# Performance work log

Measured on AMD Instinct MI355X. Metric: run time of the kernel, lower is better.

The kernel has to match this reference:

```python
import jax, jax.numpy as jnp
import numpy as np

N = 100000   # nodes per ntype
E = 1600000  # edges per etype (avg degree 16)
D = 128      # in_channels == hid_channels
LN_EPS = 1e-5


def setup_inputs() -> dict:
    key = jax.random.key(0)
    k = jax.random.split(key, 16)
    scale = 1.0 / np.sqrt(D)
    inp = {
        "x_A": jax.random.normal(k[0], (N, D), jnp.float32),
        "x_B": jax.random.normal(k[1], (N, D), jnp.float32),
        # per-etype GraphConv weights, etype order: [aa, ab, ba, bb]
        "W0": jax.random.normal(k[2], (4, D, D), jnp.float32) * scale,
        "b0": jnp.zeros((4, D), jnp.float32),
        "W1": jax.random.normal(k[3], (4, D, D), jnp.float32) * scale,
        "b1": jnp.zeros((4, D), jnp.float32),
        # LayerNorm params: [layer, ntype(A=0,B=1), D]
        "ln_gamma": jnp.ones((2, 2, D), jnp.float32),
        "ln_beta": jnp.zeros((2, 2, D), jnp.float32),
        "src_aa": jax.random.randint(k[4], (E,), 0, N, jnp.int32),
        "dst_aa": jax.random.randint(k[5], (E,), 0, N, jnp.int32),
        "src_ab": jax.random.randint(k[6], (E,), 0, N, jnp.int32),
        "dst_ab": jax.random.randint(k[7], (E,), 0, N, jnp.int32),
        "src_ba": jax.random.randint(k[8], (E,), 0, N, jnp.int32),
        "dst_ba": jax.random.randint(k[9], (E,), 0, N, jnp.int32),
        "src_bb": jax.random.randint(k[10], (E,), 0, N, jnp.int32),
        "dst_bb": jax.random.randint(k[11], (E,), 0, N, jnp.int32),
    }
    return inp


def _layer_norm(x, g, b):
    m = jnp.mean(x, axis=-1, keepdims=True)
    v = jnp.var(x, axis=-1, keepdims=True)
    return (x - m) * jax.lax.rsqrt(v + LN_EPS) * g + b


def _graph_conv(x, W, b, src, dst, n_dst, act):
    # dgl GraphConv norm='both': D_dst^{-1/2} A D_src^{-1/2} X W + b
    deg_out = jnp.clip(jax.ops.segment_sum(jnp.ones_like(src, x.dtype), src, num_segments=x.shape[0]), 1.0)
    deg_in = jnp.clip(jax.ops.segment_sum(jnp.ones_like(dst, x.dtype), dst, num_segments=n_dst), 1.0)
    h = (x * jax.lax.rsqrt(deg_out)[:, None]) @ W            # transform first (in==out)
    agg = jax.ops.segment_sum(h[src], dst, num_segments=n_dst)
    out = agg * jax.lax.rsqrt(deg_in)[:, None] + b
    return jax.nn.relu(out) if act else out


def reference(x_A, x_B, W0, b0, W1, b1, ln_gamma, ln_beta,
              src_aa, dst_aa, src_ab, dst_ab, src_ba, dst_ba, src_bb, dst_bb):
    hA, hB = x_A, x_B
    for l, (W, bias) in enumerate([(W0, b0), (W1, b1)]):
        act = (l == 0)  # relu inside each GraphConv for all but the last layer
        # HeteroGraphConv aggregate='sum': sum per-relation (activated) outputs per dst ntype
        nA = _graph_conv(hA, W[0], bias[0], src_aa, dst_aa, N, act) + \
             _graph_conv(hB, W[2], bias[2], src_ba, dst_ba, N, act)
        nB = _graph_conv(hA, W[1], bias[1], src_ab, dst_ab, N, act) + \
             _graph_conv(hB, W[3], bias[3], src_bb, dst_bb, N, act)
        hA = _layer_norm(nA, ln_gamma[l, 0], ln_beta[l, 0])
        hB = _layer_norm(nB, ln_gamma[l, 1], ln_beta[l, 1])
        # dropout p=0.0 (eval) -> identity
    return jnp.stack([hA, hB])  # [ntype, N, D]
```

## Files before the change

kernel.cpp:

```cpp
#include <hip/hip_runtime.h>
#include <hip/hip_bf16.h>

#define D 128
typedef unsigned int uint;
typedef unsigned short ushort;
typedef unsigned char uchar;
typedef short short8 __attribute__((ext_vector_type(8)));
typedef float f32x4 __attribute__((ext_vector_type(4)));

#define BKT_SHIFT 8
#define NBMAX 512
#define PART_EPT 16
#define EPB 4096
#define SCAT_CAP 8192

__device__ __forceinline__ ushort f2bf(float f) {
    uint u = __float_as_uint(f);
    return (ushort)((u + 0x7fffu + ((u >> 16) & 1u)) >> 16);
}
__device__ __forceinline__ float bf2f(uint s) { return __uint_as_float(s << 16); }

__global__ __launch_bounds__(256) void bhist4_k(
    const int* __restrict__ s0, const int* __restrict__ d0,
    const int* __restrict__ s1, const int* __restrict__ d1,
    const int* __restrict__ s2, const int* __restrict__ d2,
    const int* __restrict__ s3, const int* __restrict__ d3,
    int* __restrict__ bcs, int* __restrict__ bcd, int N, int E) {
    const int e = blockIdx.y;
    const int* sp = e == 0 ? s0 : e == 1 ? s1 : e == 2 ? s2 : s3;
    const int* dp = e == 0 ? d0 : e == 1 ? d1 : e == 2 ? d2 : d3;
    const int NB = (N + 255) >> BKT_SHIFT;
    __shared__ int hs[NBMAX], hd[NBMAX];
    for (int j = threadIdx.x; j < NBMAX; j += 256) { hs[j] = 0; hd[j] = 0; }
    __syncthreads();
    const int base = blockIdx.x * 8192;
#pragma unroll
    for (int k = 0; k < 8; ++k) {
        int idx = base + (k * 256 + threadIdx.x) * 4;
        if (idx + 4 <= E) {
            int4 s = *(const int4*)(sp + idx);
            int4 d = *(const int4*)(dp + idx);
            atomicAdd(&hs[s.x >> BKT_SHIFT], 1); atomicAdd(&hs[s.y >> BKT_SHIFT], 1);
            atomicAdd(&hs[s.z >> BKT_SHIFT], 1); atomicAdd(&hs[s.w >> BKT_SHIFT], 1);
            atomicAdd(&hd[d.x >> BKT_SHIFT], 1); atomicAdd(&hd[d.y >> BKT_SHIFT], 1);
            atomicAdd(&hd[d.z >> BKT_SHIFT], 1); atomicAdd(&hd[d.w >> BKT_SHIFT], 1);
        } else {
            for (int i = idx; i < E && i < idx + 4; ++i) {
                atomicAdd(&hs[sp[i] >> BKT_SHIFT], 1);
                atomicAdd(&hd[dp[i] >> BKT_SHIFT], 1);
            }
        }
    }
    __syncthreads();
    for (int j = threadIdx.x; j < NB; j += 256) {
        if (hs[j]) atomicAdd(&bcs[e * NBMAX + j], hs[j]);
        if (hd[j]) atomicAdd(&bcd[e * NBMAX + j], hd[j]);
    }
}

__global__ __launch_bounds__(512) void bscan_k(
    const int* __restrict__ bcs, const int* __restrict__ bcd,
    int* __restrict__ sbase, int* __restrict__ scur,
    int* __restrict__ dbase, int* __restrict__ dcur, int N) {
    const int e = blockIdx.y;
    const int side = blockIdx.x;
    const int NB = (N + 255) >> BKT_SHIFT;
    const int* in = (side ? bcd : bcs) + e * NBMAX;
    int* b0 = (side ? dbase : sbase) + e * NBMAX;
    int* c0 = (side ? dcur : scur) + e * NBMAX;
    const int tid = threadIdx.x, lane = tid & 63, wid = tid >> 6;
    int v = (tid < NB) ? in[tid] : 0;
    int x = v;
#pragma unroll
    for (int off = 1; off < 64; off <<= 1) {
        int t = __shfl_up(x, off);
        if (lane >= off) x += t;
    }
    __shared__ int ws[8];
    if (lane == 63) ws[wid] = x;
    __syncthreads();
    if (tid == 0) {
        int run = 0;
#pragma unroll
        for (int w = 0; w < 8; ++w) { int t = ws[w]; ws[w] = run; run += t; }
    }
    __syncthreads();
    int excl = ws[wid] + x - v;
    if (tid < NB) { b0[tid] = excl; c0[tid] = excl; }
}

__device__ __forceinline__ void scan_reserve(int* h, int* gcur, int* Lb, int* Gb,
                                             int* ws) {
    const int t = threadIdx.x, lane = t & 63, wid = t >> 6;
    int c0 = h[2 * t], c1 = h[2 * t + 1];
    int tsum = c0 + c1;
    int x = tsum;
#pragma unroll
    for (int off = 1; off < 64; off <<= 1) {
        int u = __shfl_up(x, off);
        if (lane >= off) x += u;
    }
    if (lane == 63) ws[wid] = x;
    __syncthreads();
    if (t == 0) {
        int run = 0;
#pragma unroll
        for (int w = 0; w < 4; ++w) { int u = ws[w]; ws[w] = run; run += u; }
    }
    __syncthreads();
    int excl = ws[wid] + x - tsum;
    Lb[2 * t] = excl;
    Lb[2 * t + 1] = excl + c0;
    Gb[2 * t] = c0 ? atomicAdd(&gcur[2 * t], c0) : 0;
    Gb[2 * t + 1] = c1 ? atomicAdd(&gcur[2 * t + 1], c1) : 0;
}

__global__ __launch_bounds__(256) void part4_k(
    const int* __restrict__ s0, const int* __restrict__ d0,
    const int* __restrict__ s1, const int* __restrict__ d1,
    const int* __restrict__ s2, const int* __restrict__ d2,
    const int* __restrict__ s3, const int* __restrict__ d3,
    int* __restrict__ scur, int* __restrict__ dcur,
    uint* __restrict__ pd, uchar* __restrict__ ps, int N, int E) {
    const int e = blockIdx.y;
    const int* sp = e == 0 ? s0 : e == 1 ? s1 : e == 2 ? s2 : s3;
    const int* dp = e == 0 ? d0 : e == 1 ? d1 : e == 2 ? d2 : d3;
    uint* ptd = pd + (size_t)e * E;
    uchar* pts = ps + (size_t)e * E;
    __shared__ int hd[NBMAX], hs[NBMAX];
    __shared__ int Lb[NBMAX], Gb[NBMAX];
    __shared__ uint rec[EPB];
    __shared__ int dst[EPB];
    __shared__ int ws[4];
    for (int j = threadIdx.x; j < NBMAX; j += 256) { hd[j] = 0; hs[j] = 0; }
    __syncthreads();
    int myd[PART_EPT], mys[PART_EPT], rkd[PART_EPT], rks[PART_EPT];
    const int base = blockIdx.x * EPB;
    const int nE = min(EPB, E - base);
#pragma unroll
    for (int k = 0; k < PART_EPT; ++k) {
        int idx = base + k * 256 + threadIdx.x;
        if (idx < E) {
            int d = dp[idx], s = sp[idx];
            myd[k] = d; mys[k] = s;
            rkd[k] = atomicAdd(&hd[d >> BKT_SHIFT], 1);
            rks[k] = atomicAdd(&hs[s >> BKT_SHIFT], 1);
        } else {
            myd[k] = -1;
        }
    }
    __syncthreads();
    scan_reserve(hd, dcur + e * NBMAX, Lb, Gb, ws);
    __syncthreads();
#pragma unroll
    for (int k = 0; k < PART_EPT; ++k) {
        if (myd[k] >= 0) {
            int b = myd[k] >> BKT_SHIFT;
            int q = Lb[b] + rkd[k];
            rec[q] = ((uint)(myd[k] & 255) << 24) | (uint)mys[k];
            dst[q] = Gb[b] + rkd[k];
        }
    }
    __syncthreads();
    for (int i = threadIdx.x; i < nE; i += 256) ptd[dst[i]] = rec[i];
    __syncthreads();
    scan_reserve(hs, scur + e * NBMAX, Lb, Gb, ws);
    __syncthreads();
#pragma unroll
    for (int k = 0; k < PART_EPT; ++k) {
        if (myd[k] >= 0) {
            int b = mys[k] >> BKT_SHIFT;
            int q = Lb[b] + rks[k];
            rec[q] = (uint)(mys[k] & 255);
            dst[q] = Gb[b] + rks[k];
        }
    }
    __syncthreads();
    for (int i = threadIdx.x; i < nE; i += 256) pts[dst[i]] = (uchar)rec[i];
}

__global__ __launch_bounds__(256) void scat4_k(
    const uint* __restrict__ pd, const int* __restrict__ dbase,
    const int* __restrict__ bcd, int* __restrict__ start_g,
    int* __restrict__ cnt_g, float* __restrict__ rs_in,
    int* __restrict__ csr, int N, int E) {
    const int e = blockIdx.y;
    const int b = blockIdx.x;
    const int node0 = b << BKT_SHIFT;
    const int nodes = min(256, N - node0);
    const uint* pt = pd + (size_t)e * E;
    int* out = csr + (size_t)e * E;
    const int csr_base = dbase[e * NBMAX + b];
    const int span = bcd[e * NBMAX + b];
    __shared__ int cnt[256];
    __shared__ int cur[256];
    __shared__ int woff[4];
    __shared__ int lcsr[SCAT_CAP];
    const int tid = threadIdx.x, lane = tid & 63, wid = tid >> 6;
    cnt[tid] = 0;
    __syncthreads();
    for (int i = tid; i < span; i += 256) atomicAdd(&cnt[pt[csr_base + i] >> 24], 1);
    __syncthreads();
    int c = cnt[tid];
    int x = c;
#pragma unroll
    for (int off = 1; off < 64; off <<= 1) {
        int t = __shfl_up(x, off);
        if (lane >= off) x += t;
    }
    if (lane == 63) woff[wid] = x;
    __syncthreads();
    if (tid == 0) {
        int run = 0;
#pragma unroll
        for (int w = 0; w < 4; ++w) { int t = woff[w]; woff[w] = run; run += t; }
    }
    __syncthreads();
    int loc = woff[wid] + x - c;
    cur[tid] = loc;
    if (tid < nodes) {
        int n = node0 + tid;
        start_g[(size_t)e * N + n] = csr_base + loc;
        cnt_g[(size_t)e * N + n] = c;
        rs_in[(size_t)e * N + n] = rsqrtf((float)max(c, 1));
    }
    __syncthreads();
    for (int i = tid; i < span; i += 256) {
        uint pk = pt[csr_base + i];
        int pos = atomicAdd(&cur[pk >> 24], 1);
        int s = (int)(pk & 0xFFFFFFu);
        if (pos < SCAT_CAP) lcsr[pos] = s;
        else out[csr_base + pos] = s;
    }
    __syncthreads();
    const int lim = span < SCAT_CAP ? span : SCAT_CAP;
    for (int i = tid; i < lim; i += 256) out[csr_base + i] = lcsr[i];
}

__global__ __launch_bounds__(256) void shist_k(
    const uchar* __restrict__ ps, const int* __restrict__ sbase,
    const int* __restrict__ bcs, float* __restrict__ rs_out, int N, int E) {
    const int e = blockIdx.y;
    const int b = blockIdx.x;
    const int node0 = b << BKT_SHIFT;
    const int nodes = min(256, N - node0);
    const uchar* pt = ps + (size_t)e * E;
    const int base = sbase[e * NBMAX + b];
    const int span = bcs[e * NBMAX + b];
    __shared__ int c[256];
    c[threadIdx.x] = 0;
    __syncthreads();
    for (int i = threadIdx.x; i < span; i += 256) atomicAdd(&c[pt[base + i]], 1);
    __syncthreads();
    if (threadIdx.x < nodes)
        rs_out[(size_t)e * N + node0 + threadIdx.x] = rsqrtf((float)max(c[threadIdx.x], 1));
}

__global__ __launch_bounds__(256) void wswz_k(const float* __restrict__ W0,
                                              const float* __restrict__ W1,
                                              ushort* __restrict__ WF) {
    int t = blockIdx.x * 256 + threadIdx.x;
    int lane = t & 63, kf = (t >> 6) & 3, ct = (t >> 8) & 7, e = (t >> 11) & 3, l = (t >> 13) & 1;
    const float* Ws = (l ? W1 : W0) + (size_t)e * D * D;
    int m = lane & 15, q = lane >> 4;
    const float* src = Ws + (size_t)(kf * 32 + q * 8) * D + ct * 16 + m;
    ushort v[8];
#pragma unroll
    for (int j = 0; j < 8; ++j) v[j] = f2bf(src[(size_t)j * D]);
    uint4 pk;
    pk.x = (uint)v[0] | ((uint)v[1] << 16);
    pk.y = (uint)v[2] | ((uint)v[3] << 16);
    pk.z = (uint)v[4] | ((uint)v[5] << 16);
    pk.w = (uint)v[6] | ((uint)v[7] << 16);
    *(uint4*)(WF + ((size_t)(l * 4 + e) * 2048 + (ct * 4 + kf) * 64 + lane) * 8) = pk;
}

__global__ __launch_bounds__(256) void gemm_pair_k(
    const float* __restrict__ XA, const float* __restrict__ XB,
    const ushort* __restrict__ WF,
    const float* __restrict__ rs,
    ushort* __restrict__ yb,
    int n) {
    const int p = blockIdx.y;
    const float* X = p ? XB : XA;
    const int e0 = 2 * p, e1 = 2 * p + 1;
    const short8* F0 = (const short8*)(WF + (size_t)e0 * 16384);
    const short8* F1 = (const short8*)(WF + (size_t)e1 * 16384);
    const float* rs0 = rs + (size_t)e0 * n;
    const float* rs1 = rs + (size_t)e1 * n;
    ushort* Y0 = yb + (size_t)e0 * n * D;
    ushort* Y1 = yb + (size_t)e1 * n * D;
    const int lane = threadIdx.x & 63;
    const int m = lane & 15, q = lane >> 4;
    const int wave = blockIdx.x * 4 + (threadIdx.x >> 6);
    const int nw = gridDim.x * 4;
    const int nstrips = (n + 15) >> 4;
    for (int sidx = wave; sidx < nstrips; sidx += nw) {
        const int r = sidx * 16 + m;
        const int rc = r < n ? r : n - 1;
        const float* xp = X + (size_t)rc * D + q * 8;
        short8 xf[4];
#pragma unroll
        for (int kf = 0; kf < 4; ++kf) {
            float4 u0 = *(const float4*)(xp + kf * 32);
            float4 u1 = *(const float4*)(xp + kf * 32 + 4);
            short8 v;
            v[0] = (short)f2bf(u0.x); v[1] = (short)f2bf(u0.y);
            v[2] = (short)f2bf(u0.z); v[3] = (short)f2bf(u0.w);
            v[4] = (short)f2bf(u1.x); v[5] = (short)f2bf(u1.y);
            v[6] = (short)f2bf(u1.z); v[7] = (short)f2bf(u1.w);
            xf[kf] = v;
        }
        f32x4 a0[8], a1[8];
#pragma unroll
        for (int ct = 0; ct < 8; ++ct) {
            a0[ct] = (f32x4){0.f, 0.f, 0.f, 0.f};
            a1[ct] = (f32x4){0.f, 0.f, 0.f, 0.f};
        }
#pragma unroll
        for (int ct = 0; ct < 8; ++ct)
#pragma unroll
            for (int kf = 0; kf < 4; ++kf) {
                a0[ct] = __builtin_amdgcn_mfma_f32_16x16x32_bf16(
                    F0[(ct * 4 + kf) * 64 + lane], xf[kf], a0[ct], 0, 0, 0);
                a1[ct] = __builtin_amdgcn_mfma_f32_16x16x32_bf16(
                    F1[(ct * 4 + kf) * 64 + lane], xf[kf], a1[ct], 0, 0, 0);
            }
        if (r < n) {
            float s0v = rs0[r], s1v = rs1[r];
            ushort* y0r = Y0 + (size_t)r * D + q * 4;
            ushort* y1r = Y1 + (size_t)r * D + q * 4;
#pragma unroll
            for (int ct = 0; ct < 8; ++ct) {
                uint2 w;
                w.x = (uint)f2bf(a0[ct][0] * s0v) | ((uint)f2bf(a0[ct][1] * s0v) << 16);
                w.y = (uint)f2bf(a0[ct][2] * s0v) | ((uint)f2bf(a0[ct][3] * s0v) << 16);
                *(uint2*)(y0r + ct * 16) = w;
                uint2 z;
                z.x = (uint)f2bf(a1[ct][0] * s1v) | ((uint)f2bf(a1[ct][1] * s1v) << 16);
                z.y = (uint)f2bf(a1[ct][2] * s1v) | ((uint)f2bf(a1[ct][3] * s1v) << 16);
                *(uint2*)(y1r + ct * 16) = z;
            }
        }
    }
}

#define ACC8(acc, u)                                                     \
    acc[0] += bf2f(u.x & 0xffffu); acc[1] += bf2f(u.x >> 16);            \
    acc[2] += bf2f(u.y & 0xffffu); acc[3] += bf2f(u.y >> 16);            \
    acc[4] += bf2f(u.z & 0xffffu); acc[5] += bf2f(u.z >> 16);            \
    acc[6] += bf2f(u.w & 0xffffu); acc[7] += bf2f(u.w >> 16);

__global__ __launch_bounds__(256) void agg_ln4_k(
    const ushort* __restrict__ yb, const int* __restrict__ csr,
    const int* __restrict__ start, const int* __restrict__ cnt,
    const float* __restrict__ rs_in, const float* __restrict__ bias,
    const float* __restrict__ lng, const float* __restrict__ lnb,
    float* __restrict__ outA, float* __restrict__ outB,
    int N, int E, int act, int layer) {
    const int dt = blockIdx.y;
    const int eA = dt, eB = dt + 2;
    const int lane = threadIdx.x & 63;
    const int grp = lane >> 4, m = lane & 15;
    const int row = blockIdx.x * 4 + (threadIdx.x >> 6);
    if (row >= N) return;
    const uint4* YA = (const uint4*)(yb + (size_t)eA * N * D);
    const uint4* YB = (const uint4*)(yb + (size_t)eB * N * D);
    const int* cAp = csr + (size_t)eA * E;
    const int* cBp = csr + (size_t)eB * E;
    int iA = start[(size_t)eA * N + row], enA = iA + cnt[(size_t)eA * N + row];
    int iB = start[(size_t)eB * N + row], enB = iB + cnt[(size_t)eB * N + row];
    float aA[8] = {0.f, 0.f, 0.f, 0.f, 0.f, 0.f, 0.f, 0.f};
    float aB[8] = {0.f, 0.f, 0.f, 0.f, 0.f, 0.f, 0.f, 0.f};
    for (; iA + 4 <= enA; iA += 4) {
        int s = cAp[iA + grp];
        uint4 u = YA[(size_t)s * 16 + m];
        ACC8(aA, u)
    }
    {
        int remA = enA - iA;
        if (grp < remA) {
            int s = cAp[iA + grp];
            uint4 u = YA[(size_t)s * 16 + m];
            ACC8(aA, u)
        }
    }
    for (; iB + 4 <= enB; iB += 4) {
        int s = cBp[iB + grp];
        uint4 u = YB[(size_t)s * 16 + m];
        ACC8(aB, u)
    }
    {
        int remB = enB - iB;
        if (grp < remB) {
            int s = cBp[iB + grp];
            uint4 u = YB[(size_t)s * 16 + m];
            ACC8(aB, u)
        }
    }
#pragma unroll
    for (int j = 0; j < 8; ++j) {
        aA[j] += __shfl_xor(aA[j], 16); aA[j] += __shfl_xor(aA[j], 32);
        aB[j] += __shfl_xor(aB[j], 16); aB[j] += __shfl_xor(aB[j], 32);
    }
    float riA = rs_in[(size_t)eA * N + row], riB = rs_in[(size_t)eB * N + row];
    float4 bA0 = *(const float4*)(bias + eA * D + m * 8);
    float4 bA1 = *(const float4*)(bias + eA * D + m * 8 + 4);
    float4 bB0 = *(const float4*)(bias + eB * D + m * 8);
    float4 bB1 = *(const float4*)(bias + eB * D + m * 8 + 4);
    float bAv[8] = {bA0.x, bA0.y, bA0.z, bA0.w, bA1.x, bA1.y, bA1.z, bA1.w};
    float bBv[8] = {bB0.x, bB0.y, bB0.z, bB0.w, bB1.x, bB1.y, bB1.z, bB1.w};
    float v[8];
#pragma unroll
    for (int j = 0; j < 8; ++j) {
        float x = fmaf(aA[j], riA, bAv[j]);
        float w = fmaf(aB[j], riB, bBv[j]);
        if (act) { x = fmaxf(x, 0.f); w = fmaxf(w, 0.f); }
        v[j] = x + w;
    }
    float s = 0.f, qq = 0.f;
#pragma unroll
    for (int j = 0; j < 8; ++j) { s += v[j]; qq += v[j] * v[j]; }
#pragma unroll
    for (int off = 1; off < 16; off <<= 1) {
        s += __shfl_xor(s, off);
        qq += __shfl_xor(qq, off);
    }
    float mean = s * (1.f / 128.f);
    float var = qq * (1.f / 128.f) - mean * mean;
    float inv = rsqrtf(var + 1e-5f);
    const int gi = (layer * 2 + dt) * D + m * 8;
    float4 g0 = *(const float4*)(lng + gi);
    float4 g1 = *(const float4*)(lng + gi + 4);
    float4 be0 = *(const float4*)(lnb + gi);
    float4 be1 = *(const float4*)(lnb + gi + 4);
    float gv[8] = {g0.x, g0.y, g0.z, g0.w, g1.x, g1.y, g1.z, g1.w};
    float bev[8] = {be0.x, be0.y, be0.z, be0.w, be1.x, be1.y, be1.z, be1.w};
    if (grp == 0) {
        float4 o0, o1;
        o0.x = fmaf((v[0] - mean) * inv, gv[0], bev[0]);
        o0.y = fmaf((v[1] - mean) * inv, gv[1], bev[1]);
        o0.z = fmaf((v[2] - mean) * inv, gv[2], bev[2]);
        o0.w = fmaf((v[3] - mean) * inv, gv[3], bev[3]);
        o1.x = fmaf((v[4] - mean) * inv, gv[4], bev[4]);
        o1.y = fmaf((v[5] - mean) * inv, gv[5], bev[5]);
        o1.z = fmaf((v[6] - mean) * inv, gv[6], bev[6]);
        o1.w = fmaf((v[7] - mean) * inv, gv[7], bev[7]);
        float* OUT = dt ? outB : outA;
        *(float4*)(OUT + (size_t)row * D + m * 8) = o0;
        *(float4*)(OUT + (size_t)row * D + m * 8 + 4) = o1;
    }
}

extern "C" void kernel_launch(void* const* d_in, const int* in_sizes, int n_in,
                              void* d_out, int out_size, void* d_ws, size_t ws_size,
                              hipStream_t stream) {
    const int N = in_sizes[0] / D;
    const int E = in_sizes[8];
    const float* xA = (const float*)d_in[0];
    const float* xB = (const float*)d_in[1];
    const float* W0 = (const float*)d_in[2];
    const float* b0 = (const float*)d_in[3];
    const float* W1 = (const float*)d_in[4];
    const float* b1 = (const float*)d_in[5];
    const float* lng = (const float*)d_in[6];
    const float* lnb = (const float*)d_in[7];
    const int* s_aa = (const int*)d_in[8];
    const int* d_aa = (const int*)d_in[9];
    const int* s_ab = (const int*)d_in[10];
    const int* d_ab = (const int*)d_in[11];
    const int* s_ba = (const int*)d_in[12];
    const int* d_ba = (const int*)d_in[13];
    const int* s_bb = (const int*)d_in[14];
    const int* d_bb = (const int*)d_in[15];

    const size_t nd = (size_t)N * D;
    char* p = (char*)d_ws;
    ushort* y = (ushort*)p;
    p += 4 * nd * sizeof(ushort);
    ushort* WF = (ushort*)p;
    p += 2 * 4 * 2048 * 8 * sizeof(ushort);
    int* bcnt_s = (int*)p;
    int* bcnt_d = bcnt_s + 4 * NBMAX;
    int* sbase = bcnt_d + 4 * NBMAX;
    int* scur = sbase + 4 * NBMAX;
    int* dbase = scur + 4 * NBMAX;
    int* dcur = dbase + 4 * NBMAX;
    int* start_g = dcur + 4 * NBMAX;
    int* cnt_g = start_g + 4 * (size_t)N;
    p = (char*)(cnt_g + 4 * (size_t)N);
    float* rs_out = (float*)p;
    float* rs_in = rs_out + 4 * (size_t)N;
    p = (char*)(rs_in + 4 * (size_t)N);
    int* csr = (int*)p;
    uint* part_d = (uint*)y;
    uchar* part_s = (uchar*)(part_d + 4 * (size_t)E);

    float* hA = (float*)d_out;
    float* hB = hA + nd;

    hipMemsetAsync(bcnt_s, 0, 2 * 4 * NBMAX * sizeof(int), stream);

    const int TB = 256;
    const int NBn = (N + 255) >> BKT_SHIFT;

    dim3 bhg((E + 8191) / 8192, 4);
    bhist4_k<<<bhg, TB, 0, stream>>>(s_aa, d_aa, s_ab, d_ab, s_ba, d_ba, s_bb, d_bb,
                                     bcnt_s, bcnt_d, N, E);
    dim3 bsg(2, 4);
    bscan_k<<<bsg, 512, 0, stream>>>(bcnt_s, bcnt_d, sbase, scur, dbase, dcur, N);
    dim3 pg4((E + EPB - 1) / EPB, 4);
    part4_k<<<pg4, TB, 0, stream>>>(s_aa, d_aa, s_ab, d_ab, s_ba, d_ba, s_bb, d_bb,
                                    scur, dcur, part_d, part_s, N, E);
    dim3 scg4(NBn, 4);
    scat4_k<<<scg4, TB, 0, stream>>>(part_d, dbase, bcnt_d, start_g, cnt_g, rs_in,
                                     csr, N, E);
    shist_k<<<scg4, TB, 0, stream>>>(part_s, sbase, bcnt_s, rs_out, N, E);
    wswz_k<<<64, TB, 0, stream>>>(W0, W1, WF);

    dim3 gg(384, 2);
    dim3 ag((N + 3) / 4, 2);
    const size_t WFL = 4 * 2048 * 8;

    gemm_pair_k<<<gg, TB, 0, stream>>>(xA, xB, WF, rs_out, y, N);
    agg_ln4_k<<<ag, TB, 0, stream>>>(y, csr, start_g, cnt_g, rs_in, b0,
                                     lng, lnb, hA, hB, N, E, 1, 0);
    gemm_pair_k<<<gg, TB, 0, stream>>>(hA, hB, WF + WFL, rs_out, y, N);
    agg_ln4_k<<<ag, TB, 0, stream>>>(y, csr, start_g, cnt_g, rs_in, b1,
                                     lng, lnb, hA, hB, N, E, 0, 1);
}
```

Before: 977.2 us.

## Aggregate bf16 features before transform and fuse GEMM with bias, ReLU and LayerNorm

Reorders each GraphConv layer to gather and sum the bf16 source features first, scaled per edge by the source normalisation. A GEMM then follows, with bias, ReLU, the cross-relation sum and LayerNorm fused into its epilogue. Gathers now read two compact bf16 node tables instead of four transformed ones, which should improve cache hit rates for the random gathers. Layer 0 writes its output as bf16 for reuse by the next layer's gather instead of fp32. The cost is an extra per-edge scale lookup, a new input cast kernel, and a separate per-relation aggregate buffer that the GEMM must read back.

```diff
diff --git a/kernel.cpp b/kernel.cpp
--- a/kernel.cpp
+++ b/kernel.cpp
@@ -19,6 +19,22 @@
     return (ushort)((u + 0x7fffu + ((u >> 16) & 1u)) >> 16);
 }
 __device__ __forceinline__ float bf2f(uint s) { return __uint_as_float(s << 16); }
+
+__global__ __launch_bounds__(256) void cast2_k(const float* __restrict__ A,
+                                               const float* __restrict__ B,
+                                               ushort* __restrict__ xb, int nd8) {
+    int i = blockIdx.x * 256 + threadIdx.x;
+    if (i >= 2 * nd8) return;
+    const float* src = (i < nd8) ? (A + (size_t)i * 8) : (B + (size_t)(i - nd8) * 8);
+    float4 u0 = *(const float4*)src;
+    float4 u1 = *(const float4*)(src + 4);
+    uint4 pk;
+    pk.x = (uint)f2bf(u0.x) | ((uint)f2bf(u0.y) << 16);
+    pk.y = (uint)f2bf(u0.z) | ((uint)f2bf(u0.w) << 16);
+    pk.z = (uint)f2bf(u1.x) | ((uint)f2bf(u1.y) << 16);
+    pk.w = (uint)f2bf(u1.z) | ((uint)f2bf(u1.w) << 16);
+    *(uint4*)(xb + (size_t)i * 8) = pk;
+}
 
 __global__ __launch_bounds__(256) void bhist4_k(
     const int* __restrict__ s0, const int* __restrict__ d0,
@@ -275,21 +291,97 @@
     *(uint4*)(WF + ((size_t)(l * 4 + e) * 2048 + (ct * 4 + kf) * 64 + lane) * 8) = pk;
 }
 
-__global__ __launch_bounds__(256) void gemm_pair_k(
-    const float* __restrict__ XA, const float* __restrict__ XB,
-    const ushort* __restrict__ WF,
-    const float* __restrict__ rs,
-    ushort* __restrict__ yb,
-    int n) {
+__global__ __launch_bounds__(256) void agg4_k(
+    const ushort* __restrict__ xb, const int* __restrict__ csr,
+    const int* __restrict__ start, const int* __restrict__ cnt,
+    const float* __restrict__ rs_out, const float* __restrict__ rs_in,
+    ushort* __restrict__ agg, int N, int E) {
+    const int dt = blockIdx.y;
+    const int eA = dt, eB = dt + 2;
+    const int lane = threadIdx.x & 63;
+    const int row = blockIdx.x * 4 + (threadIdx.x >> 6);
+    if (row >= N) return;
+    const size_t nd = (size_t)N * D;
+    const uint* XA = (const uint*)xb;
+    const uint* XB = (const uint*)(xb + nd);
+    const float* roA = rs_out + (size_t)eA * N;
+    const float* roB = rs_out + (size_t)eB * N;
+    const int* cAp = csr + (size_t)eA * E;
+    const int* cBp = csr + (size_t)eB * E;
+    int iA = start[(size_t)eA * N + row], enA = iA + cnt[(size_t)eA * N + row];
+    int iB = start[(size_t)eB * N + row], enB = iB + cnt[(size_t)eB * N + row];
+    float a0 = 0.f, a1 = 0.f, c0 = 0.f, c1 = 0.f;
+    while (iA + 4 <= enA && iB + 4 <= enB) {
+        int sa0 = cAp[iA], sa1 = cAp[iA + 1], sa2 = cAp[iA + 2], sa3 = cAp[iA + 3];
+        int sb0 = cBp[iB], sb1 = cBp[iB + 1], sb2 = cBp[iB + 2], sb3 = cBp[iB + 3];
+        float ra0 = roA[sa0], ra1 = roA[sa1], ra2 = roA[sa2], ra3 = roA[sa3];
+        float rb0 = roB[sb0], rb1 = roB[sb1], rb2 = roB[sb2], rb3 = roB[sb3];
+        uint pa0 = XA[(size_t)sa0 * 64 + lane], pa1 = XA[(size_t)sa1 * 64 + lane];
+        uint pa2 = XA[(size_t)sa2 * 64 + lane], pa3 = XA[(size_t)sa3 * 64 + lane];
+        uint pb0 = XB[(size_t)sb0 * 64 + lane], pb1 = XB[(size_t)sb1 * 64 + lane];
+        uint pb2 = XB[(size_t)sb2 * 64 + lane], pb3 = XB[(size_t)sb3 * 64 + lane];
+        a0 = fmaf(bf2f(pa0 & 0xffffu), ra0, a0); a1 = fmaf(bf2f(pa0 >> 16), ra0, a1);
+        a0 = fmaf(bf2f(pa1 & 0xffffu), ra1, a0); a1 = fmaf(bf2f(pa1 >> 16), ra1, a1);
+        a0 = fmaf(bf2f(pa2 & 0xffffu), ra2, a0); a1 = fmaf(bf2f(pa2 >> 16), ra2, a1);
+        a0 = fmaf(bf2f(pa3 & 0xffffu), ra3, a0); a1 = fmaf(bf2f(pa3 >> 16), ra3, a1);
+        c0 = fmaf(bf2f(pb0 & 0xffffu), rb0, c0); c1 = fmaf(bf2f(pb0 >> 16), rb0, c1);
+        c0 = fmaf(bf2f(pb1 & 0xffffu), rb1, c0); c1 = fmaf(bf2f(pb1 >> 16), rb1, c1);
+        c0 = fmaf(bf2f(pb2 & 0xffffu), rb2, c0); c1 = fmaf(bf2f(pb2 >> 16), rb2, c1);
+        c0 = fmaf(bf2f(pb3 & 0xffffu), rb3, c0); c1 = fmaf(bf2f(pb3 >> 16), rb3, c1);
+        iA += 4; iB += 4;
+    }
+    for (; iA + 4 <= enA; iA += 4) {
+        int s0 = cAp[iA], s1 = cAp[iA + 1], s2 = cAp[iA + 2], s3 = cAp[iA + 3];
+        float r0 = roA[s0], r1 = roA[s1], r2 = roA[s2], r3 = roA[s3];
+        uint p0 = XA[(size_t)s0 * 64 + lane], p1 = XA[(size_t)s1 * 64 + lane];
+        uint p2 = XA[(size_t)s2 * 64 + lane], p3 = XA[(size_t)s3 * 64 + lane];
+        a0 = fmaf(bf2f(p0 & 0xffffu), r0, a0); a1 = fmaf(bf2f(p0 >> 16), r0, a1);
+        a0 = fmaf(bf2f(p1 & 0xffffu), r1, a0); a1 = fmaf(bf2f(p1 >> 16), r1, a1);
+        a0 = fmaf(bf2f(p2 & 0xffffu), r2, a0); a1 = fmaf(bf2f(p2 >> 16), r2, a1);
+        a0 = fmaf(bf2f(p3 & 0xffffu), r3, a0); a1 = fmaf(bf2f(p3 >> 16), r3, a1);
+    }
+    for (; iB + 4 <= enB; iB += 4) {
+        int s0 = cBp[iB], s1 = cBp[iB + 1], s2 = cBp[iB + 2], s3 = cBp[iB + 3];
+        float r0 = roB[s0], r1 = roB[s1], r2 = roB[s2], r3 = roB[s3];
+        uint p0 = XB[(size_t)s0 * 64 + lane], p1 = XB[(size_t)s1 * 64 + lane];
+        uint p2 = XB[(size_t)s2 * 64 + lane], p3 = XB[(size_t)s3 * 64 + lane];
+        c0 = fmaf(bf2f(p0 & 0xffffu), r0, c0); c1 = fmaf(bf2f(p0 >> 16), r0, c1);
+        c0 = fmaf(bf2f(p1 & 0xffffu), r1, c0); c1 = fmaf(bf2f(p1 >> 16), r1, c1);
+        c0 = fmaf(bf2f(p2 & 0xffffu), r2, c0); c1 = fmaf(bf2f(p2 >> 16), r2, c1);
+        c0 = fmaf(bf2f(p3 & 0xffffu), r3, c0); c1 = fmaf(bf2f(p3 >> 16), r3, c1);
+    }
+    for (; iA < enA; ++iA) {
+        int s = cAp[iA];
+        float r = roA[s];
+        uint p = XA[(size_t)s * 64 + lane];
+        a0 = fmaf(bf2f(p & 0xffffu), r, a0); a1 = fmaf(bf2f(p >> 16), r, a1);
+    }
+    for (; iB < enB; ++iB) {
+        int s = cBp[iB];
+        float r = roB[s];
+        uint p = XB[(size_t)s * 64 + lane];
+        c0 = fmaf(bf2f(p & 0xffffu), r, c0); c1 = fmaf(bf2f(p >> 16), r, c1);
+    }
+    float riA = rs_in[(size_t)eA * N + row], riB = rs_in[(size_t)eB * N + row];
+    uint* agU = (uint*)agg;
+    agU[((size_t)eA * N + row) * 64 + lane] =
+        (uint)f2bf(a0 * riA) | ((uint)f2bf(a1 * riA) << 16);
+    agU[((size_t)eB * N + row) * 64 + lane] =
+        (uint)f2bf(c0 * riB) | ((uint)f2bf(c1 * riB) << 16);
+}
+
+__global__ __launch_bounds__(256) void gemm_ln_k(
+    const ushort* __restrict__ AGG, const ushort* __restrict__ WF,
+    const float* __restrict__ bias, const float* __restrict__ lng,
+    const float* __restrict__ lnb, ushort* __restrict__ xb_out,
+    float* __restrict__ outA, float* __restrict__ outB,
+    int n, int layer, int act) {
     const int p = blockIdx.y;
-    const float* X = p ? XB : XA;
-    const int e0 = 2 * p, e1 = 2 * p + 1;
+    const int e0 = p, e1 = p + 2;
     const short8* F0 = (const short8*)(WF + (size_t)e0 * 16384);
     const short8* F1 = (const short8*)(WF + (size_t)e1 * 16384);
-    const float* rs0 = rs + (size_t)e0 * n;
-    const float* rs1 = rs + (size_t)e1 * n;
-    ushort* Y0 = yb + (size_t)e0 * n * D;
-    ushort* Y1 = yb + (size_t)e1 * n * D;
+    const ushort* A0 = AGG + (size_t)e0 * n * D;
+    const ushort* A1 = AGG + (size_t)e1 * n * D;
     const int lane = threadIdx.x & 63;
     const int m = lane & 15, q = lane >> 4;
     const int wave = blockIdx.x * 4 + (threadIdx.x >> 6);
@@ -298,18 +390,13 @@
     for (int sidx = wave; sidx < nstrips; sidx += nw) {
         const int r = sidx * 16 + m;
         const int rc = r < n ? r : n - 1;
-        const float* xp = X + (size_t)rc * D + q * 8;
-        short8 xf[4];
+        const ushort* xpA = A0 + (size_t)rc * D + q * 8;
+        const ushort* xpB = A1 + (size_t)rc * D + q * 8;
+        short8 xa[4], xv[4];
 #pragma unroll
         for (int kf = 0; kf < 4; ++kf) {
-            float4 u0 = *(const float4*)(xp + kf * 32);
-            float4 u1 = *(const float4*)(xp + kf * 32 + 4);
-            short8 v;
-            v[0] = (short)f2bf(u0.x); v[1] = (short)f2bf(u0.y);
-            v[2] = (short)f2bf(u0.z); v[3] = (short)f2bf(u0.w);
-            v[4] = (short)f2bf(u1.x); v[5] = (short)f2bf(u1.y);
-            v[6] = (short)f2bf(u1.z); v[7] = (short)f2bf(u1.w);
-            xf[kf] = v;
+            xa[kf] = *(const short8*)(xpA + kf * 32);
+            xv[kf] = *(const short8*)(xpB + kf * 32);
         }
         f32x4 a0[8], a1[8];
 #pragma unroll
@@ -322,133 +409,67 @@
 #pragma unroll
             for (int kf = 0; kf < 4; ++kf) {
                 a0[ct] = __builtin_amdgcn_mfma_f32_16x16x32_bf16(
-                    F0[(ct * 4 + kf) * 64 + lane], xf[kf], a0[ct], 0, 0, 0);
+                    F0[(ct * 4 + kf) * 64 + lane], xa[kf], a0[ct], 0, 0, 0);
                 a1[ct] = __builtin_amdgcn_mfma_f32_16x16x32_bf16(
-                    F1[(ct * 4 + kf) * 64 + lane], xf[kf], a1[ct], 0, 0, 0);
+                    F1[(ct * 4 + kf) * 64 + lane], xv[kf], a1[ct], 0, 0, 0);
             }
         if (r < n) {
-            float s0v = rs0[r], s1v = rs1[r];
-            ushort* y0r = Y0 + (size_t)r * D + q * 4;
-            ushort* y1r = Y1 + (size_t)r * D + q * 4;
+            float s = 0.f, qq = 0.f;
 #pragma unroll
             for (int ct = 0; ct < 8; ++ct) {
-                uint2 w;
-                w.x = (uint)f2bf(a0[ct][0] * s0v) | ((uint)f2bf(a0[ct][1] * s0v) << 16);
-                w.y = (uint)f2bf(a0[ct][2] * s0v) | ((uint)f2bf(a0[ct][3] * s0v) << 16);
-                *(uint2*)(y0r + ct * 16) = w;
-                uint2 z;
-                z.x = (uint)f2bf(a1[ct][0] * s1v) | ((uint)f2bf(a1[ct][1] * s1v) << 16);
-                z.y = (uint)f2bf(a1[ct][2] * s1v) | ((uint)f2bf(a1[ct][3] * s1v) << 16);
-                *(uint2*)(y1r + ct * 16) = z;
+                float4 bA = *(const float4*)(bias + e0 * D + ct * 16 + q * 4);
+                float4 bB = *(const float4*)(bias + e1 * D + ct * 16 + q * 4);
+                float x0 = a0[ct][0] + bA.x, w0 = a1[ct][0] + bB.x;
+                float x1 = a0[ct][1] + bA.y, w1 = a1[ct][1] + bB.y;
+                float x2 = a0[ct][2] + bA.z, w2 = a1[ct][2] + bB.z;
+                float x3 = a0[ct][3] + bA.w, w3 = a1[ct][3] + bB.w;
+                if (act) {
+                    x0 = fmaxf(x0, 0.f); x1 = fmaxf(x1, 0.f);
+                    x2 = fmaxf(x2, 0.f); x3 = fmaxf(x3, 0.f);
+                    w0 = fmaxf(w0, 0.f); w1 = fmaxf(w1, 0.f);
+                    w2 = fmaxf(w2, 0.f); w3 = fmaxf(w3, 0.f);
+                }
+                float v0 = x0 + w0, v1 = x1 + w1, v2 = x2 + w2, v3 = x3 + w3;
+                a0[ct][0] = v0; a0[ct][1] = v1; a0[ct][2] = v2; a0[ct][3] = v3;
+                s += v0 + v1 + v2 + v3;
+                qq += v0 * v0 + v1 * v1 + v2 * v2 + v3 * v3;
             }
-        }
-    }
-}
-
-#define ACC8(acc, u)                                                     \
-    acc[0] += bf2f(u.x & 0xffffu); acc[1] += bf2f(u.x >> 16);            \
-    acc[2] += bf2f(u.y & 0xffffu); acc[3] += bf2f(u.y >> 16);            \
-    acc[4] += bf2f(u.z & 0xffffu); acc[5] += bf2f(u.z >> 16);            \
-    acc[6] += bf2f(u.w & 0xffffu); acc[7] += bf2f(u.w >> 16);
-
-__global__ __launch_bounds__(256) void agg_ln4_k(
-    const ushort* __restrict__ yb, const int* __restrict__ csr,
-    const int* __restrict__ start, const int* __restrict__ cnt,
-    const float* __restrict__ rs_in, const float* __restrict__ bias,
-    const float* __restrict__ lng, const float* __restrict__ lnb,
-    float* __restrict__ outA, float* __restrict__ outB,
-    int N, int E, int act, int layer) {
-    const int dt = blockIdx.y;
-    const int eA = dt, eB = dt + 2;
-    const int lane = threadIdx.x & 63;
-    const int grp = lane >> 4, m = lane & 15;
-    const int row = blockIdx.x * 4 + (threadIdx.x >> 6);
-    if (row >= N) return;
-    const uint4* YA = (const uint4*)(yb + (size_t)eA * N * D);
-    const uint4* YB = (const uint4*)(yb + (size_t)eB * N * D);
-    const int* cAp = csr + (size_t)eA * E;
-    const int* cBp = csr + (size_t)eB * E;
-    int iA = start[(size_t)eA * N + row], enA = iA + cnt[(size_t)eA * N + row];
-    int iB = start[(size_t)eB * N + row], enB = iB + cnt[(size_t)eB * N + row];
-    float aA[8] = {0.f, 0.f, 0.f, 0.f, 0.f, 0.f, 0.f, 0.f};
-    float aB[8] = {0.f, 0.f, 0.f, 0.f, 0.f, 0.f, 0.f, 0.f};
-    for (; iA + 4 <= enA; iA += 4) {
-        int s = cAp[iA + grp];
-        uint4 u = YA[(size_t)s * 16 + m];
-        ACC8(aA, u)
-    }
-    {
-        int remA = enA - iA;
-        if (grp < remA) {
-            int s = cAp[iA + grp];
-            uint4 u = YA[(size_t)s * 16 + m];
-            ACC8(aA, u)
-        }
-    }
-    for (; iB + 4 <= enB; iB += 4) {
-        int s = cBp[iB + grp];
-        uint4 u = YB[(size_t)s * 16 + m];
-        ACC8(aB, u)
-    }
-    {
-        int remB = enB - iB;
-        if (grp < remB) {
-            int s = cBp[iB + grp];
-            uint4 u = YB[(size_t)s * 16 + m];
-            ACC8(aB, u)
-        }
-    }
-#pragma unroll
-    for (int j = 0; j < 8; ++j) {
-        aA[j] += __shfl_xor(aA[j], 16); aA[j] += __shfl_xor(aA[j], 32);
-        aB[j] += __shfl_xor(aB[j], 16); aB[j] += __shfl_xor(aB[j], 32);
-    }
-    float riA = rs_in[(size_t)eA * N + row], riB = rs_in[(size_t)eB * N + row];
-    float4 bA0 = *(const float4*)(bias + eA * D + m * 8);
-    float4 bA1 = *(const float4*)(bias + eA * D + m * 8 + 4);
-    float4 bB0 = *(const float4*)(bias + eB * D + m * 8);
-    float4 bB1 = *(const float4*)(bias + eB * D + m * 8 + 4);
-    float bAv[8] = {bA0.x, bA0.y, bA0.z, bA0.w, bA1.x, bA1.y, bA1.z, bA1.w};
-    float bBv[8] = {bB0.x, bB0.y, bB0.z, bB0.w, bB1.x, bB1.y, bB1.z, bB1.w};
-    float v[8];
-#pragma unroll
-    for (int j = 0; j < 8; ++j) {
-        float x = fmaf(aA[j], riA, bAv[j]);
-        float w = fmaf(aB[j], riB, bBv[j]);
-        if (act) { x = fmaxf(x, 0.f); w = fmaxf(w, 0.f); }
-        v[j] = x + w;
-    }
-    float s = 0.f, qq = 0.f;
-#pragma unroll
-    for (int j = 0; j < 8; ++j) { s += v[j]; qq += v[j] * v[j]; }
-#pragma unroll
-    for (int off = 1; off < 16; off <<= 1) {
-        s += __shfl_xor(s, off);
-        qq += __shfl_xor(qq, off);
-    }
-    float mean = s * (1.f / 128.f);
-    float var = qq * (1.f / 128.f) - mean * mean;
-    float inv = rsqrtf(var + 1e-5f);
-    const int gi = (layer * 2 + dt) * D + m * 8;
-    float4 g0 = *(const float4*)(lng + gi);
-    float4 g1 = *(const float4*)(lng + gi + 4);
-    float4 be0 = *(const float4*)(lnb + gi);
-    float4 be1 = *(const float4*)(lnb + gi + 4);
-    float gv[8] = {g0.x, g0.y, g0.z, g0.w, g1.x, g1.y, g1.z, g1.w};
-    float bev[8] = {be0.x, be0.y, be0.z, be0.w, be1.x, be1.y, be1.z, be1.w};
-    if (grp == 0) {
-        float4 o0, o1;
-        o0.x = fmaf((v[0] - mean) * inv, gv[0], bev[0]);
-        o0.y = fmaf((v[1] - mean) * inv, gv[1], bev[1]);
-        o0.z = fmaf((v[2] - mean) * inv, gv[2], bev[2]);
-        o0.w = fmaf((v[3] - mean) * inv, gv[3], bev[3]);
-        o1.x = fmaf((v[4] - mean) * inv, gv[4], bev[4]);
-        o1.y = fmaf((v[5] - mean) * inv, gv[5], bev[5]);
-        o1.z = fmaf((v[6] - mean) * inv, gv[6], bev[6]);
-        o1.w = fmaf((v[7] - mean) * inv, gv[7], bev[7]);
-        float* OUT = dt ? outB : outA;
-        *(float4*)(OUT + (size_t)row * D + m * 8) = o0;
-        *(float4*)(OUT + (size_t)row * D + m * 8 + 4) = o1;
+            s += __shfl_xor(s, 16); s += __shfl_xor(s, 32);
+            qq += __shfl_xor(qq, 16); qq += __shfl_xor(qq, 32);
+            float mean = s * (1.f / 128.f);
+            float var = qq * (1.f / 128.f) - mean * mean;
+            float inv = rsqrtf(var + 1e-5f);
+            const int gbase = (layer * 2 + p) * D;
+            if (layer == 0) {
+                ushort* yr = xb_out + (size_t)p * n * D + (size_t)r * D + q * 4;
+#pragma unroll
+                for (int ct = 0; ct < 8; ++ct) {
+                    float4 g = *(const float4*)(lng + gbase + ct * 16 + q * 4);
+                    float4 be = *(const float4*)(lnb + gbase + ct * 16 + q * 4);
+                    float o0 = fmaf((a0[ct][0] - mean) * inv, g.x, be.x);
+                    float o1 = fmaf((a0[ct][1] - mean) * inv, g.y, be.y);
+                    float o2 = fmaf((a0[ct][2] - mean) * inv, g.z, be.z);
+                    float o3 = fmaf((a0[ct][3] - mean) * inv, g.w, be.w);
+                    uint2 wv;
+                    wv.x = (uint)f2bf(o0) | ((uint)f2bf(o1) << 16);
+                    wv.y = (uint)f2bf(o2) | ((uint)f2bf(o3) << 16);
+                    *(uint2*)(yr + ct * 16) = wv;
+                }
+            } else {
+                float* OUT = (p ? outB : outA) + (size_t)r * D + q * 4;
+#pragma unroll
+                for (int ct = 0; ct < 8; ++ct) {
+                    float4 g = *(const float4*)(lng + gbase + ct * 16 + q * 4);
+                    float4 be = *(const float4*)(lnb + gbase + ct * 16 + q * 4);
+                    float4 o;
+                    o.x = fmaf((a0[ct][0] - mean) * inv, g.x, be.x);
+                    o.y = fmaf((a0[ct][1] - mean) * inv, g.y, be.y);
+                    o.z = fmaf((a0[ct][2] - mean) * inv, g.z, be.z);
+                    o.w = fmaf((a0[ct][3] - mean) * inv, g.w, be.w);
+                    *(float4*)(OUT + ct * 16) = o;
+                }
+            }
+        }
     }
 }
 
@@ -476,7 +497,9 @@
 
     const size_t nd = (size_t)N * D;
     char* p = (char*)d_ws;
-    ushort* y = (ushort*)p;
+    ushort* xb = (ushort*)p;
+    p += 2 * nd * sizeof(ushort);
+    ushort* agg = (ushort*)p;
     p += 4 * nd * sizeof(ushort);
     ushort* WF = (ushort*)p;
     p += 2 * 4 * 2048 * 8 * sizeof(ushort);
@@ -493,7 +516,7 @@
     float* rs_in = rs_out + 4 * (size_t)N;
     p = (char*)(rs_in + 4 * (size_t)N);
     int* csr = (int*)p;
-    uint* part_d = (uint*)y;
+    uint* part_d = (uint*)agg;
     uchar* part_s = (uchar*)(part_d + 4 * (size_t)E);
 
     float* hA = (float*)d_out;
@@ -503,7 +526,9 @@
 
     const int TB = 256;
     const int NBn = (N + 255) >> BKT_SHIFT;
-
+    const int nd8 = (int)(nd / 8);
+
+    cast2_k<<<(2 * nd8 + 255) / 256, TB, 0, stream>>>(xA, xB, xb, nd8);
     dim3 bhg((E + 8191) / 8192, 4);
     bhist4_k<<<bhg, TB, 0, stream>>>(s_aa, d_aa, s_ab, d_ab, s_ba, d_ba, s_bb, d_bb,
                                      bcnt_s, bcnt_d, N, E);
@@ -522,10 +547,9 @@
     dim3 ag((N + 3) / 4, 2);
     const size_t WFL = 4 * 2048 * 8;
 
-    gemm_pair_k<<<gg, TB, 0, stream>>>(xA, xB, WF, rs_out, y, N);
-    agg_ln4_k<<<ag, TB, 0, stream>>>(y, csr, start_g, cnt_g, rs_in, b0,
-                                     lng, lnb, hA, hB, N, E, 1, 0);
-    gemm_pair_k<<<gg, TB, 0, stream>>>(hA, hB, WF + WFL, rs_out, y, N);
-    agg_ln4_k<<<ag, TB, 0, stream>>>(y, csr, start_g, cnt_g, rs_in, b1,
-                                     lng, lnb, hA, hB, N, E, 0, 1);
-}
+    agg4_k<<<ag, TB, 0, stream>>>(xb, csr, start_g, cnt_g, rs_out, rs_in, agg, N, E);
+    gemm_ln_k<<<gg, TB, 0, stream>>>(agg, WF, b0, lng, lnb, xb, hA, hB, N, 0, 1);
+    agg4_k<<<ag, TB, 0, stream>>>(xb, csr, start_g, cnt_g, rs_out, rs_in, agg, N, E);
+    gemm_ln_k<<<gg, TB, 0, stream>>>(agg, WF + WFL, b1, lng, lnb, (ushort*)0, hA, hB,
+                                     N, 1, 0);
+}
```

New measurement: 1.013 ms. +3.7%, slower.
